# Kernel optimization log

Measured on AMD Instinct MI355X. Metric: run time of the kernel, lower is better.

Reference implementation:

```python
import jax, jax.numpy as jnp
import numpy as np
from jax import lax

B, T, I, H = 4096, 128, 16, 64


def setup_inputs() -> dict:
    key = jax.random.key(0)
    ks = jax.random.split(key, 7)
    s_ih = 1.0 / np.sqrt(H)
    return {
        "x": jax.random.normal(ks[0], (B, T, I), dtype=jnp.float32),
        "w_ih": jax.random.uniform(ks[1], (3 * H, I), jnp.float32, -s_ih, s_ih),
        "w_hh": jax.random.uniform(ks[2], (3 * H, H), jnp.float32, -s_ih, s_ih),
        "b_ih": jax.random.uniform(ks[3], (3 * H,), jnp.float32, -s_ih, s_ih),
        "b_hh": jax.random.uniform(ks[4], (3 * H,), jnp.float32, -s_ih, s_ih),
        "fc_w": jax.random.uniform(ks[5], (1, H), jnp.float32, -s_ih, s_ih),
        "fc_b": jax.random.uniform(ks[6], (1,), jnp.float32, -s_ih, s_ih),
    }


def reference(x, w_ih, w_hh, b_ih, b_hh, fc_w, fc_b):
    # x: [B, T, I]. PyTorch GRU gate order: r, z, n.
    # Precompute input contributions to all gates for all timesteps: [B, T, 3H]
    xg = jnp.einsum('bti,gi->btg', x, w_ih) + b_ih

    def step(h, xg_t):
        # xg_t: [B, 3H], h: [B, H]
        gi_r, gi_z, gi_n = jnp.split(xg_t, 3, axis=-1)
        hg = h @ w_hh.T + b_hh  # [B, 3H]
        hr, hz, hn = jnp.split(hg, 3, axis=-1)
        r = jax.nn.sigmoid(gi_r + hr)
        z = jax.nn.sigmoid(gi_z + hz)
        n = jnp.tanh(gi_n + r * hn)
        h_new = (1.0 - z) * n + z * h
        return h_new, None

    h0 = jnp.zeros((x.shape[0], w_hh.shape[1]), dtype=x.dtype)
    hT, _ = lax.scan(step, h0, jnp.swapaxes(xg, 0, 1))  # scan over time

    # Final-step linear head, squeeze to [B]
    pred = hT @ fc_w.T + fc_b  # [B, 1]
    return pred.squeeze(-1)
```

## Files before the change

### kernel.cpp

```cpp
#include <hip/hip_runtime.h>
#include <stdint.h>


#define T_STEPS 128
#define NI 16
#define NH 64
#define RB 16

typedef float    f32x4  __attribute__((ext_vector_type(4)));
typedef uint32_t u32x4  __attribute__((ext_vector_type(4)));
typedef short    bf16x8 __attribute__((ext_vector_type(8)));
typedef __bf16   bfv8   __attribute__((ext_vector_type(8)));

static __device__ __forceinline__ uint32_t fbits(float f) { return __builtin_bit_cast(uint32_t, f); }
static __device__ __forceinline__ float    bitsf(uint32_t u) { return __builtin_bit_cast(float, u); }

static __device__ __forceinline__ float sigm_f(float x) {
  float e = __builtin_amdgcn_exp2f(-1.44269504f * x);
  return __builtin_amdgcn_rcpf(1.0f + e);
}
static __device__ __forceinline__ float tanh_f(float x) {
  float e = __builtin_amdgcn_exp2f(2.88539008f * x);
  return 1.0f - 2.0f * __builtin_amdgcn_rcpf(e + 1.0f);
}

static __device__ __forceinline__ int h_addr(int row, int col) {
  return row * 128 + (((col >> 3) ^ (row & 7)) << 4) + ((col & 7) << 1);
}

static __device__ __forceinline__ bf16x8 ld_frag16(const unsigned char* p) {
  u32x4 v = *(const u32x4*)p;
  return __builtin_bit_cast(bf16x8, v);
}

#define MFMA(acc, a, b) acc = __builtin_amdgcn_mfma_f32_16x16x32_bf16(a, b, acc, 0, 0, 0)

__global__ __launch_bounds__(256)
void gru_fused(const float* __restrict__ x,
               const float* __restrict__ w_ih,
               const float* __restrict__ w_hh,
               const float* __restrict__ b_ih,
               const float* __restrict__ b_hh,
               const float* __restrict__ fc_w,
               const float* __restrict__ fc_b,
               float* __restrict__ out)
{
  __shared__ __align__(16) unsigned char sH[2][2][2048];
  __shared__ float s_red[4][16];

  const int tid  = threadIdx.x;
  const int lane = tid & 63;
  const int wv   = tid >> 6;
  const int colg = lane & 15;
  const int grp  = lane >> 4;
  const int rb   = blockIdx.x * RB;
  const int hc   = wv * 16 + colg;

  {
    uint32_t* p = (uint32_t*)&sH[0][0][0];
    #pragma unroll
    for (int i = 0; i < 4; ++i) p[tid + 256 * i] = 0u;
  }

  bf16x8 bhi[3][2], blo[3][2], bx[3];
  #pragma unroll
  for (int g = 0; g < 3; ++g) {
    const float* wr = w_hh + (size_t)(g * 64 + hc) * NH + grp * 8;
    #pragma unroll
    for (int kt = 0; kt < 2; ++kt) {
      bfv8 vhi, vlo;
      #pragma unroll
      for (int j = 0; j < 8; ++j) {
        float w = wr[kt * 32 + j];
        __bf16 hi = (__bf16)w;
        vhi[j] = hi;
        vlo[j] = (__bf16)(w - (float)hi);
      }
      bhi[g][kt] = __builtin_bit_cast(bf16x8, vhi);
      blo[g][kt] = __builtin_bit_cast(bf16x8, vlo);
    }
    const float* wi = w_ih + (size_t)(g * 64 + hc) * NI + (grp & 1) * 8;
    bfv8 vx;
    #pragma unroll
    for (int j = 0; j < 8; ++j) vx[j] = (__bf16)wi[j];
    bx[g] = __builtin_bit_cast(bf16x8, vx);
  }

  const float bR  = b_ih[hc]       + b_hh[hc];
  const float bZ  = b_ih[64 + hc]  + b_hh[64 + hc];
  const float bNx = b_ih[128 + hc];
  const float bNh = b_hh[128 + hc];

  const float* xp = x + (size_t)(rb + colg) * T_STEPS * NI + (grp & 1) * 8;

  const int a_off0 = h_addr(colg, 0 * 32 + grp * 8);
  const int a_off1 = h_addr(colg, 1 * 32 + grp * 8);

  float hreg[4] = {0.f, 0.f, 0.f, 0.f};

  f32x4 xa = *(const f32x4*)(xp);
  f32x4 xb = *(const f32x4*)(xp + 4);

  const bool hi_grp = (grp < 2);

  __syncthreads();

  for (int t = 0; t < T_STEPS; ++t) {
    const int tn = (t < T_STEPS - 1) ? (t + 1) : t;
    f32x4 xna = *(const f32x4*)(xp + (size_t)tn * NI);
    f32x4 xnb = *(const f32x4*)(xp + (size_t)tn * NI + 4);

    const unsigned char* bh = &sH[t & 1][0][0];
    bf16x8 ah0 = ld_frag16(bh + a_off0);
    bf16x8 ah1 = ld_frag16(bh + a_off1);
    bf16x8 al0 = ld_frag16(bh + 2048 + a_off0);
    bf16x8 al1 = ld_frag16(bh + 2048 + a_off1);

    uint32_t d0, d1, d2, d3;
    {
      float v[8];
      #pragma unroll
      for (int j = 0; j < 4; ++j) {
        float x0 = xa[j], x1 = xb[j];
        float b0 = bitsf(fbits(x0) & 0xffff0000u);
        float b1 = bitsf(fbits(x1) & 0xffff0000u);
        v[j]     = hi_grp ? x0 : (x0 - b0);
        v[4 + j] = hi_grp ? x1 : (x1 - b1);
      }
      d0 = __builtin_amdgcn_perm(fbits(v[1]), fbits(v[0]), 0x07060302u);
      d1 = __builtin_amdgcn_perm(fbits(v[3]), fbits(v[2]), 0x07060302u);
      d2 = __builtin_amdgcn_perm(fbits(v[5]), fbits(v[4]), 0x07060302u);
      d3 = __builtin_amdgcn_perm(fbits(v[7]), fbits(v[6]), 0x07060302u);
    }
    u32x4 axu = {d0, d1, d2, d3};
    bf16x8 ax = __builtin_bit_cast(bf16x8, axu);

    f32x4 aR  = {0.f, 0.f, 0.f, 0.f};
    f32x4 aZ  = {0.f, 0.f, 0.f, 0.f};
    f32x4 aNh = {0.f, 0.f, 0.f, 0.f};
    f32x4 aNx = {0.f, 0.f, 0.f, 0.f};

    MFMA(aR, ah0, bhi[0][0]); MFMA(aR, ah1, bhi[0][1]);
    MFMA(aR, al0, bhi[0][0]); MFMA(aR, al1, bhi[0][1]);
    MFMA(aR, ah0, blo[0][0]); MFMA(aR, ah1, blo[0][1]);
    MFMA(aR, ax, bx[0]);

    MFMA(aZ, ah0, bhi[1][0]); MFMA(aZ, ah1, bhi[1][1]);
    MFMA(aZ, al0, bhi[1][0]); MFMA(aZ, al1, bhi[1][1]);
    MFMA(aZ, ah0, blo[1][0]); MFMA(aZ, ah1, blo[1][1]);
    MFMA(aZ, ax, bx[1]);

    MFMA(aNh, ah0, bhi[2][0]); MFMA(aNh, ah1, bhi[2][1]);
    MFMA(aNh, al0, bhi[2][0]); MFMA(aNh, al1, bhi[2][1]);
    MFMA(aNh, ah0, blo[2][0]); MFMA(aNh, ah1, blo[2][1]);
    MFMA(aNx, ax, bx[2]);

    unsigned char* bo = &sH[(t + 1) & 1][0][0];
    #pragma unroll
    for (int q = 0; q < 4; ++q) {
      float r = sigm_f(aR[q] + bR);
      float z = sigm_f(aZ[q] + bZ);
      float n = tanh_f(fmaf(r, aNh[q] + bNh, aNx[q] + bNx));
      float h = n + z * (hreg[q] - n);
      hreg[q] = h;
      int off = h_addr(grp * 4 + q, hc);
      uint32_t u = fbits(h);
      float hif = bitsf(u & 0xffff0000u);
      *(uint16_t*)(bo + off)        = (uint16_t)(u >> 16);
      *(uint16_t*)(bo + 2048 + off) = (uint16_t)(fbits(h - hif) >> 16);
    }
    __syncthreads();
    xa = xna; xb = xnb;
  }

  float fw = fc_w[hc];
  float v0 = hreg[0] * fw, v1 = hreg[1] * fw, v2 = hreg[2] * fw, v3 = hreg[3] * fw;
  #pragma unroll
  for (int off = 1; off < 16; off <<= 1) {
    v0 += __shfl_xor(v0, off, 64);
    v1 += __shfl_xor(v1, off, 64);
    v2 += __shfl_xor(v2, off, 64);
    v3 += __shfl_xor(v3, off, 64);
  }
  if (colg == 0) {
    s_red[wv][grp * 4 + 0] = v0;
    s_red[wv][grp * 4 + 1] = v1;
    s_red[wv][grp * 4 + 2] = v2;
    s_red[wv][grp * 4 + 3] = v3;
  }
  __syncthreads();
  if (tid < 16) {
    out[rb + tid] = s_red[0][tid] + s_red[1][tid] + s_red[2][tid] + s_red[3][tid] + fc_b[0];
  }
}

extern "C" void kernel_launch(void* const* d_in, const int* in_sizes, int n_in,
                              void* d_out, int out_size, void* d_ws, size_t ws_size,
                              hipStream_t stream) {
  (void)in_sizes; (void)n_in; (void)d_ws; (void)ws_size;
  const float* x    = (const float*)d_in[0];
  const float* w_ih = (const float*)d_in[1];
  const float* w_hh = (const float*)d_in[2];
  const float* b_ih = (const float*)d_in[3];
  const float* b_hh = (const float*)d_in[4];
  const float* fc_w = (const float*)d_in[5];
  const float* fc_b = (const float*)d_in[6];
  float* out = (float*)d_out;
  const int nblocks = out_size / RB;
  gru_fused<<<dim3(nblocks), dim3(256), 0, stream>>>(x, w_ih, w_hh, b_ih, b_hh,
                                                     fc_w, fc_b, out);
}
```

Before: 169.9 us.

## Split GRU hidden-K reduction across two wave halves with LDS partial-sum exchange

The block grows to 512 threads, and the K=64 hidden reduction is split across two groups of four waves. Each wave does half the MFMAs and writes partial gate sums to a padded LDS exchange buffer; after a barrier each lane combines partials and computes two of the output rows' gates. The log2e scaling is folded into the weights and biases, and the biases seed the accumulators. The h buffer drops double buffering, which adds a second barrier per timestep, and the exchange adds LDS traffic in exchange for shorter MFMA chains per wave.

```diff
diff --git a/kernel.cpp b/kernel.cpp
--- a/kernel.cpp
+++ b/kernel.cpp
@@ -6,23 +6,18 @@
 #define NI 16
 #define NH 64
 #define RB 16
+#define S_EX 20
+#define PLANE (16 * S_EX)
 
 typedef float    f32x4  __attribute__((ext_vector_type(4)));
 typedef uint32_t u32x4  __attribute__((ext_vector_type(4)));
 typedef short    bf16x8 __attribute__((ext_vector_type(8)));
 typedef __bf16   bfv8   __attribute__((ext_vector_type(8)));
 
+static constexpr float LOG2E = 1.4426950408889634f;
+
 static __device__ __forceinline__ uint32_t fbits(float f) { return __builtin_bit_cast(uint32_t, f); }
 static __device__ __forceinline__ float    bitsf(uint32_t u) { return __builtin_bit_cast(float, u); }
-
-static __device__ __forceinline__ float sigm_f(float x) {
-  float e = __builtin_amdgcn_exp2f(-1.44269504f * x);
-  return __builtin_amdgcn_rcpf(1.0f + e);
-}
-static __device__ __forceinline__ float tanh_f(float x) {
-  float e = __builtin_amdgcn_exp2f(2.88539008f * x);
-  return 1.0f - 2.0f * __builtin_amdgcn_rcpf(e + 1.0f);
-}
 
 static __device__ __forceinline__ int h_addr(int row, int col) {
   return row * 128 + (((col >> 3) ^ (row & 7)) << 4) + ((col & 7) << 1);
@@ -35,7 +30,7 @@
 
 #define MFMA(acc, a, b) acc = __builtin_amdgcn_mfma_f32_16x16x32_bf16(a, b, acc, 0, 0, 0)
 
-__global__ __launch_bounds__(256)
+__global__ __launch_bounds__(512)
 void gru_fused(const float* __restrict__ x,
                const float* __restrict__ w_ih,
                const float* __restrict__ w_hh,
@@ -45,152 +40,187 @@
                const float* __restrict__ fc_b,
                float* __restrict__ out)
 {
-  __shared__ __align__(16) unsigned char sH[2][2][2048];
-  __shared__ float s_red[4][16];
+  __shared__ __align__(16) unsigned char sH[2][2048];
+  __shared__ __align__(16) float sEx[4][8][PLANE];
+  __shared__ float s_red[8][8];
 
   const int tid  = threadIdx.x;
   const int lane = tid & 63;
   const int wv   = tid >> 6;
+  const int pair = wv & 3;
+  const int kh   = wv >> 2;
   const int colg = lane & 15;
   const int grp  = lane >> 4;
   const int rb   = blockIdx.x * RB;
-  const int hc   = wv * 16 + colg;
-
-  {
-    uint32_t* p = (uint32_t*)&sH[0][0][0];
-    #pragma unroll
-    for (int i = 0; i < 4; ++i) p[tid + 256 * i] = 0u;
-  }
-
-  bf16x8 bhi[3][2], blo[3][2], bx[3];
+  const int hc   = pair * 16 + colg;
+
+  ((uint32_t*)sH)[tid]       = 0u;
+  ((uint32_t*)sH)[tid + 512] = 0u;
+
+  const float scl0 = -LOG2E, scl2 = 2.0f * LOG2E;
+  bf16x8 bhi[3], blo[3];
   #pragma unroll
   for (int g = 0; g < 3; ++g) {
-    const float* wr = w_hh + (size_t)(g * 64 + hc) * NH + grp * 8;
+    const float s = (g == 2) ? scl2 : scl0;
+    const float* wr = w_hh + (size_t)(g * 64 + hc) * NH + kh * 32 + grp * 8;
+    bfv8 vhi, vlo;
     #pragma unroll
-    for (int kt = 0; kt < 2; ++kt) {
-      bfv8 vhi, vlo;
+    for (int j = 0; j < 8; ++j) {
+      float w = wr[j] * s;
+      __bf16 hi = (__bf16)w;
+      vhi[j] = hi;
+      vlo[j] = (__bf16)(w - (float)hi);
+    }
+    bhi[g] = __builtin_bit_cast(bf16x8, vhi);
+    blo[g] = __builtin_bit_cast(bf16x8, vlo);
+  }
+  bf16x8 bx[3];
+  if (kh) {
+    #pragma unroll
+    for (int g = 0; g < 3; ++g) {
+      const float s = (g == 2) ? scl2 : scl0;
+      const float* wi = w_ih + (size_t)(g * 64 + hc) * NI + (grp & 1) * 8;
+      bfv8 vx;
       #pragma unroll
-      for (int j = 0; j < 8; ++j) {
-        float w = wr[kt * 32 + j];
-        __bf16 hi = (__bf16)w;
-        vhi[j] = hi;
-        vlo[j] = (__bf16)(w - (float)hi);
+      for (int j = 0; j < 8; ++j) vx[j] = (__bf16)(wi[j] * s);
+      bx[g] = __builtin_bit_cast(bf16x8, vx);
+    }
+  }
+
+  const float biasR  = kh ? scl0 * (b_ih[hc] + b_hh[hc])           : 0.f;
+  const float biasZ  = kh ? scl0 * (b_ih[64 + hc] + b_hh[64 + hc]) : 0.f;
+  const float biasNh = kh ? scl2 * b_hh[128 + hc]                  : 0.f;
+  const float biasNx = kh ? scl2 * b_ih[128 + hc]                  : 0.f;
+
+  const int a_hi = h_addr(colg, kh * 32 + grp * 8);
+  const int a_lo = 2048 + a_hi;
+  const int wo0  = h_addr(kh * 8 + 2 * grp + 0, hc);
+  const int wo1  = h_addr(kh * 8 + 2 * grp + 1, hc);
+  float* exW = &sEx[pair][kh * 4][(4 * grp) * S_EX + colg];
+  const float* exR = &sEx[pair][0][(kh * 8 + 2 * grp) * S_EX + colg];
+
+  float hold0 = 0.f, hold1 = 0.f;
+
+  const float* xp = x + (size_t)(rb + colg) * T_STEPS * NI + (grp & 1) * 8;
+  f32x4 xa = {0.f,0.f,0.f,0.f}, xb = {0.f,0.f,0.f,0.f};
+  if (kh) { xa = *(const f32x4*)xp; xb = *(const f32x4*)(xp + 4); }
+  const bool hi_grp = (grp < 2);
+
+  __syncthreads();
+
+  for (int t = 0; t < T_STEPS; ++t) {
+    bf16x8 ah = ld_frag16((const unsigned char*)sH + a_hi);
+    bf16x8 al = ld_frag16((const unsigned char*)sH + a_lo);
+
+    f32x4 aR  = {biasR,  biasR,  biasR,  biasR};
+    f32x4 aZ  = {biasZ,  biasZ,  biasZ,  biasZ};
+    f32x4 aNh = {biasNh, biasNh, biasNh, biasNh};
+    f32x4 aNx = {biasNx, biasNx, biasNx, biasNx};
+
+    bf16x8 ax;
+    f32x4 xna = xa, xnb = xb;
+    if (kh) {
+      uint32_t d0, d1, d2, d3;
+      {
+        float v[8];
+        #pragma unroll
+        for (int j = 0; j < 4; ++j) {
+          float x0 = xa[j], x1 = xb[j];
+          float b0 = bitsf(fbits(x0) & 0xffff0000u);
+          float b1 = bitsf(fbits(x1) & 0xffff0000u);
+          v[j]     = hi_grp ? x0 : (x0 - b0);
+          v[4 + j] = hi_grp ? x1 : (x1 - b1);
+        }
+        d0 = __builtin_amdgcn_perm(fbits(v[1]), fbits(v[0]), 0x07060302u);
+        d1 = __builtin_amdgcn_perm(fbits(v[3]), fbits(v[2]), 0x07060302u);
+        d2 = __builtin_amdgcn_perm(fbits(v[5]), fbits(v[4]), 0x07060302u);
+        d3 = __builtin_amdgcn_perm(fbits(v[7]), fbits(v[6]), 0x07060302u);
       }
-      bhi[g][kt] = __builtin_bit_cast(bf16x8, vhi);
-      blo[g][kt] = __builtin_bit_cast(bf16x8, vlo);
-    }
-    const float* wi = w_ih + (size_t)(g * 64 + hc) * NI + (grp & 1) * 8;
-    bfv8 vx;
-    #pragma unroll
-    for (int j = 0; j < 8; ++j) vx[j] = (__bf16)wi[j];
-    bx[g] = __builtin_bit_cast(bf16x8, vx);
-  }
-
-  const float bR  = b_ih[hc]       + b_hh[hc];
-  const float bZ  = b_ih[64 + hc]  + b_hh[64 + hc];
-  const float bNx = b_ih[128 + hc];
-  const float bNh = b_hh[128 + hc];
-
-  const float* xp = x + (size_t)(rb + colg) * T_STEPS * NI + (grp & 1) * 8;
-
-  const int a_off0 = h_addr(colg, 0 * 32 + grp * 8);
-  const int a_off1 = h_addr(colg, 1 * 32 + grp * 8);
-
-  float hreg[4] = {0.f, 0.f, 0.f, 0.f};
-
-  f32x4 xa = *(const f32x4*)(xp);
-  f32x4 xb = *(const f32x4*)(xp + 4);
-
-  const bool hi_grp = (grp < 2);
-
-  __syncthreads();
-
-  for (int t = 0; t < T_STEPS; ++t) {
-    const int tn = (t < T_STEPS - 1) ? (t + 1) : t;
-    f32x4 xna = *(const f32x4*)(xp + (size_t)tn * NI);
-    f32x4 xnb = *(const f32x4*)(xp + (size_t)tn * NI + 4);
-
-    const unsigned char* bh = &sH[t & 1][0][0];
-    bf16x8 ah0 = ld_frag16(bh + a_off0);
-    bf16x8 ah1 = ld_frag16(bh + a_off1);
-    bf16x8 al0 = ld_frag16(bh + 2048 + a_off0);
-    bf16x8 al1 = ld_frag16(bh + 2048 + a_off1);
-
-    uint32_t d0, d1, d2, d3;
-    {
-      float v[8];
-      #pragma unroll
-      for (int j = 0; j < 4; ++j) {
-        float x0 = xa[j], x1 = xb[j];
-        float b0 = bitsf(fbits(x0) & 0xffff0000u);
-        float b1 = bitsf(fbits(x1) & 0xffff0000u);
-        v[j]     = hi_grp ? x0 : (x0 - b0);
-        v[4 + j] = hi_grp ? x1 : (x1 - b1);
-      }
-      d0 = __builtin_amdgcn_perm(fbits(v[1]), fbits(v[0]), 0x07060302u);
-      d1 = __builtin_amdgcn_perm(fbits(v[3]), fbits(v[2]), 0x07060302u);
-      d2 = __builtin_amdgcn_perm(fbits(v[5]), fbits(v[4]), 0x07060302u);
-      d3 = __builtin_amdgcn_perm(fbits(v[7]), fbits(v[6]), 0x07060302u);
-    }
-    u32x4 axu = {d0, d1, d2, d3};
-    bf16x8 ax = __builtin_bit_cast(bf16x8, axu);
-
-    f32x4 aR  = {0.f, 0.f, 0.f, 0.f};
-    f32x4 aZ  = {0.f, 0.f, 0.f, 0.f};
-    f32x4 aNh = {0.f, 0.f, 0.f, 0.f};
-    f32x4 aNx = {0.f, 0.f, 0.f, 0.f};
-
-    MFMA(aR, ah0, bhi[0][0]); MFMA(aR, ah1, bhi[0][1]);
-    MFMA(aR, al0, bhi[0][0]); MFMA(aR, al1, bhi[0][1]);
-    MFMA(aR, ah0, blo[0][0]); MFMA(aR, ah1, blo[0][1]);
-    MFMA(aR, ax, bx[0]);
-
-    MFMA(aZ, ah0, bhi[1][0]); MFMA(aZ, ah1, bhi[1][1]);
-    MFMA(aZ, al0, bhi[1][0]); MFMA(aZ, al1, bhi[1][1]);
-    MFMA(aZ, ah0, blo[1][0]); MFMA(aZ, ah1, blo[1][1]);
-    MFMA(aZ, ax, bx[1]);
-
-    MFMA(aNh, ah0, bhi[2][0]); MFMA(aNh, ah1, bhi[2][1]);
-    MFMA(aNh, al0, bhi[2][0]); MFMA(aNh, al1, bhi[2][1]);
-    MFMA(aNh, ah0, blo[2][0]); MFMA(aNh, ah1, blo[2][1]);
-    MFMA(aNx, ax, bx[2]);
-
-    unsigned char* bo = &sH[(t + 1) & 1][0][0];
+      u32x4 axu = {d0, d1, d2, d3};
+      ax = __builtin_bit_cast(bf16x8, axu);
+      const int tn = (t < T_STEPS - 1) ? (t + 1) : t;
+      xna = *(const f32x4*)(xp + (size_t)tn * NI);
+      xnb = *(const f32x4*)(xp + (size_t)tn * NI + 4);
+    }
+
+    MFMA(aR,  ah, bhi[0]); MFMA(aR,  al, bhi[0]); MFMA(aR,  ah, blo[0]);
+    MFMA(aZ,  ah, bhi[1]); MFMA(aZ,  al, bhi[1]); MFMA(aZ,  ah, blo[1]);
+    MFMA(aNh, ah, bhi[2]); MFMA(aNh, al, bhi[2]); MFMA(aNh, ah, blo[2]);
+    if (kh) {
+      MFMA(aR,  ax, bx[0]);
+      MFMA(aZ,  ax, bx[1]);
+      MFMA(aNx, ax, bx[2]);
+    }
+
     #pragma unroll
     for (int q = 0; q < 4; ++q) {
-      float r = sigm_f(aR[q] + bR);
-      float z = sigm_f(aZ[q] + bZ);
-      float n = tanh_f(fmaf(r, aNh[q] + bNh, aNx[q] + bNx));
-      float h = n + z * (hreg[q] - n);
-      hreg[q] = h;
-      int off = h_addr(grp * 4 + q, hc);
+      exW[q * S_EX + 0 * PLANE] = aR[q];
+      exW[q * S_EX + 1 * PLANE] = aZ[q];
+      exW[q * S_EX + 2 * PLANE] = aNh[q];
+    }
+    if (kh) {
+      #pragma unroll
+      for (int q = 0; q < 4; ++q) exW[q * S_EX + 3 * PLANE] = aNx[q];
+    }
+    __syncthreads();
+
+    {
+      float sRv = exR[0 * S_EX + 0 * PLANE] + exR[0 * S_EX + 4 * PLANE];
+      float sZv = exR[0 * S_EX + 1 * PLANE] + exR[0 * S_EX + 5 * PLANE];
+      float sNh = exR[0 * S_EX + 2 * PLANE] + exR[0 * S_EX + 6 * PLANE];
+      float sNx = exR[0 * S_EX + 7 * PLANE];
+      float r = __builtin_amdgcn_rcpf(1.0f + __builtin_amdgcn_exp2f(sRv));
+      float z = __builtin_amdgcn_rcpf(1.0f + __builtin_amdgcn_exp2f(sZv));
+      float tv = fmaf(r, sNh, sNx);
+      float n = fmaf(-2.0f, __builtin_amdgcn_rcpf(__builtin_amdgcn_exp2f(tv) + 1.0f), 1.0f);
+      float h = n + z * (hold0 - n);
+      hold0 = h;
       uint32_t u = fbits(h);
       float hif = bitsf(u & 0xffff0000u);
-      *(uint16_t*)(bo + off)        = (uint16_t)(u >> 16);
-      *(uint16_t*)(bo + 2048 + off) = (uint16_t)(fbits(h - hif) >> 16);
+      *(uint16_t*)((unsigned char*)sH + wo0)        = (uint16_t)(u >> 16);
+      *(uint16_t*)((unsigned char*)sH + 2048 + wo0) = (uint16_t)(fbits(h - hif) >> 16);
+    }
+    {
+      float sRv = exR[1 * S_EX + 0 * PLANE] + exR[1 * S_EX + 4 * PLANE];
+      float sZv = exR[1 * S_EX + 1 * PLANE] + exR[1 * S_EX + 5 * PLANE];
+      float sNh = exR[1 * S_EX + 2 * PLANE] + exR[1 * S_EX + 6 * PLANE];
+      float sNx = exR[1 * S_EX + 7 * PLANE];
+      float r = __builtin_amdgcn_rcpf(1.0f + __builtin_amdgcn_exp2f(sRv));
+      float z = __builtin_amdgcn_rcpf(1.0f + __builtin_amdgcn_exp2f(sZv));
+      float tv = fmaf(r, sNh, sNx);
+      float n = fmaf(-2.0f, __builtin_amdgcn_rcpf(__builtin_amdgcn_exp2f(tv) + 1.0f), 1.0f);
+      float h = n + z * (hold1 - n);
+      hold1 = h;
+      uint32_t u = fbits(h);
+      float hif = bitsf(u & 0xffff0000u);
+      *(uint16_t*)((unsigned char*)sH + wo1)        = (uint16_t)(u >> 16);
+      *(uint16_t*)((unsigned char*)sH + 2048 + wo1) = (uint16_t)(fbits(h - hif) >> 16);
     }
     __syncthreads();
     xa = xna; xb = xnb;
   }
 
   float fw = fc_w[hc];
-  float v0 = hreg[0] * fw, v1 = hreg[1] * fw, v2 = hreg[2] * fw, v3 = hreg[3] * fw;
+  float v0 = hold0 * fw, v1 = hold1 * fw;
   #pragma unroll
   for (int off = 1; off < 16; off <<= 1) {
     v0 += __shfl_xor(v0, off, 64);
     v1 += __shfl_xor(v1, off, 64);
-    v2 += __shfl_xor(v2, off, 64);
-    v3 += __shfl_xor(v3, off, 64);
   }
   if (colg == 0) {
-    s_red[wv][grp * 4 + 0] = v0;
-    s_red[wv][grp * 4 + 1] = v1;
-    s_red[wv][grp * 4 + 2] = v2;
-    s_red[wv][grp * 4 + 3] = v3;
+    s_red[wv][2 * grp + 0] = v0;
+    s_red[wv][2 * grp + 1] = v1;
   }
   __syncthreads();
   if (tid < 16) {
-    out[rb + tid] = s_red[0][tid] + s_red[1][tid] + s_red[2][tid] + s_red[3][tid] + fc_b[0];
+    float s = fc_b[0];
+    if (tid < 8) {
+      s += s_red[0][tid] + s_red[1][tid] + s_red[2][tid] + s_red[3][tid];
+    } else {
+      int r2 = tid - 8;
+      s += s_red[4][r2] + s_red[5][r2] + s_red[6][r2] + s_red[7][r2];
+    }
+    out[rb + tid] = s;
   }
 }
 
@@ -207,6 +237,6 @@
   const float* fc_b = (const float*)d_in[6];
   float* out = (float*)d_out;
   const int nblocks = out_size / RB;
-  gru_fused<<<dim3(nblocks), dim3(256), 0, stream>>>(x, w_ih, w_hh, b_ih, b_hh,
+  gru_fused<<<dim3(nblocks), dim3(512), 0, stream>>>(x, w_ih, w_hh, b_ih, b_hh,
                                                      fc_w, fc_b, out);
 }
```

After: 173.8 us. +2.3%, slower.
